# Optimization experiments

Hardware: AMD Instinct MI355X
Metric: run time of the kernel (lower is better)

The kernel has to match this reference:

```python
import jax, jax.numpy as jnp
import numpy as np

N_NODES = 50000
N_EDGES = 800000
N_GRAPHS = 512
IN_DIM = 128
HIDDEN = 64
N_CLASSES = 2


def gcn_conv(x, W, b, src, dst, n_nodes):
    """PyG GCNConv: add self-loops, symmetric deg^-1/2 normalization,
    linear transform then scatter-add aggregation at the target nodes."""
    xw = x @ W  # [N, out]
    loop = jnp.arange(n_nodes)
    s = jnp.concatenate([src, loop])  # sources incl. self-loops
    d = jnp.concatenate([dst, loop])  # targets incl. self-loops
    deg = jax.ops.segment_sum(jnp.ones(s.shape, xw.dtype), d, num_segments=n_nodes)
    dinv = jax.lax.rsqrt(jnp.where(deg > 0, deg, 1.0))
    norm = dinv[s] * dinv[d]  # [E+N]
    out = jax.ops.segment_sum(xw[s] * norm[:, None], d, num_segments=n_nodes)
    return out + b


def setup_inputs() -> dict:
    key = jax.random.key(0)
    ks = jax.random.split(key, 9)
    x = jax.random.normal(ks[0], (N_NODES, IN_DIM), dtype=jnp.float32)
    edge_index = jax.random.randint(ks[1], (2, N_EDGES), 0, N_NODES)
    batch = jnp.sort(jax.random.randint(ks[2], (N_NODES,), 0, N_GRAPHS))
    def glorot(k, fi, fo):
        return jax.random.normal(k, (fi, fo), dtype=jnp.float32) * (1.0 / np.sqrt(fi))
    W1 = glorot(ks[3], IN_DIM, HIDDEN)
    W2 = glorot(ks[4], HIDDEN, HIDDEN)
    W3 = glorot(ks[5], HIDDEN, N_CLASSES)
    b1 = jnp.zeros((HIDDEN,), jnp.float32)
    b2 = jnp.zeros((HIDDEN,), jnp.float32)
    b3 = jnp.zeros((N_CLASSES,), jnp.float32)
    return {"x": x, "edge_index": edge_index, "batch": batch,
            "W1": W1, "b1": b1, "W2": W2, "b2": b2, "W3": W3, "b3": b3}


def reference(x, edge_index, batch, W1, b1, W2, b2, W3, b3):
    # Eval mode: F.dropout(training=False) is identity.
    src, dst = edge_index[0], edge_index[1]
    z = jax.nn.relu(gcn_conv(x, W1, b1, src, dst, N_NODES))
    z = jax.nn.relu(gcn_conv(z, W2, b2, src, dst, N_NODES))
    z = gcn_conv(z, W3, b3, src, dst, N_NODES)  # [N, 2]
    # global_mean_pool over graph ids (only the last pooling result is returned)
    s = jax.ops.segment_sum(z, batch, num_segments=N_GRAPHS)
    cnt = jax.ops.segment_sum(jnp.ones((N_NODES,), z.dtype), batch, num_segments=N_GRAPHS)
    return s / jnp.clip(cnt, 1.0)[:, None]
```

## Files before the change

kernel.cpp:

```cpp
#include <hip/hip_runtime.h>
#include <hip/hip_bf16.h>

#define N_NODES   50000
#define N_EDGES   800000
#define N_GRAPHS  512
#define IN_DIM    128
#define HIDDEN    64
#define NPAD      50176
#define NBLK      196
#define SHARD_BLOCKS 1024

__global__ __launch_bounds__(256) void k_degi_sh(const int* __restrict__ dst,
                                                 int* __restrict__ degi) {
    const int shard = blockIdx.x & 7;
    const int blk   = blockIdx.x >> 3;
    const int nthr  = (SHARD_BLOCKS >> 3) * 256;
    for (int e = blk * 256 + threadIdx.x; e < N_EDGES; e += nthr) {
        int d = dst[e];
        if (((d >> 4) & 7) == shard) atomicAdd(&degi[d], 1);
    }
}

__global__ __launch_bounds__(256) void k_dinv(const int* __restrict__ degi,
                                              float* __restrict__ dinv) {
    int i = blockIdx.x * 256 + threadIdx.x;
    if (i < N_NODES) dinv[i] = rsqrtf((float)degi[i] + 1.0f);
}

__global__ __launch_bounds__(256) void k_scan_block(const int* __restrict__ degi,
                                                    int* __restrict__ offs,
                                                    int* __restrict__ bsum) {
    __shared__ int sh[256];
    int tid = threadIdx.x;
    int i = blockIdx.x * 256 + tid;
    int v = degi[i];
    sh[tid] = v;
    __syncthreads();
    #pragma unroll
    for (int off = 1; off < 256; off <<= 1) {
        int t = (tid >= off) ? sh[tid - off] : 0;
        __syncthreads();
        sh[tid] += t;
        __syncthreads();
    }
    offs[i] = sh[tid] - v;
    if (tid == 255) bsum[blockIdx.x] = sh[tid];
}

__global__ __launch_bounds__(256) void k_scan_bsum(int* __restrict__ bsum,
                                                   int* __restrict__ boff) {
    __shared__ int sh[256];
    int tid = threadIdx.x;
    int v = (tid < NBLK) ? bsum[tid] : 0;
    sh[tid] = v;
    __syncthreads();
    #pragma unroll
    for (int off = 1; off < 256; off <<= 1) {
        int t = (tid >= off) ? sh[tid - off] : 0;
        __syncthreads();
        sh[tid] += t;
        __syncthreads();
    }
    if (tid < NBLK) boff[tid] = sh[tid] - v;
}

__global__ __launch_bounds__(256) void k_scan_add(int* __restrict__ offs,
                                                  const int* __restrict__ boff,
                                                  int* __restrict__ cnt) {
    int i = blockIdx.x * 256 + threadIdx.x;
    int v = offs[i] + boff[blockIdx.x];
    offs[i] = v;
    cnt[i]  = v;
}

__global__ __launch_bounds__(256) void k_fill_sh(const int* __restrict__ src,
                                                 const int* __restrict__ dst,
                                                 int* __restrict__ cnt,
                                                 int* __restrict__ csr_src) {
    const int shard = blockIdx.x & 7;
    const int blk   = blockIdx.x >> 3;
    const int nthr  = (SHARD_BLOCKS >> 3) * 256;
    for (int e = blk * 256 + threadIdx.x; e < N_EDGES; e += nthr) {
        int d = dst[e];
        int s = src[e];
        if (((d >> 4) & 7) == shard) {
            int pos = atomicAdd(&cnt[d], 1);
            csr_src[pos] = s;
        }
    }
}

template <int K, bool RELU_IN>
__global__ __launch_bounds__(256) void k_gemm64t(const float* __restrict__ A,
                                                 const float* __restrict__ W,
                                                 const float* __restrict__ bin,
                                                 const float* __restrict__ dinv,
                                                 float* __restrict__ out) {
    __shared__ float sA[64][65];
    __shared__ float sW[64][64];
    __shared__ float sB[64];

    const int tid = threadIdx.x;
    const int rowBase = blockIdx.x * 64;
    const int c0 = (tid & 15) * 4;
    const int r0 = (tid >> 4) * 4;

    if (RELU_IN && tid < 64) sB[tid] = bin[tid];

    float acc[4][4];
    #pragma unroll
    for (int j = 0; j < 4; ++j)
        #pragma unroll
        for (int c = 0; c < 4; ++c) acc[j][c] = 0.0f;

    for (int kc = 0; kc < K; kc += 64) {
        __syncthreads();
        #pragma unroll
        for (int p = 0; p < 4; ++p) {
            int i = p * 256 + tid;
            int k  = i >> 4;
            int cq = i & 15;
            *reinterpret_cast<float4*>(&sW[k][cq * 4]) =
                *reinterpret_cast<const float4*>(&W[(size_t)(kc + k) * 64 + cq * 4]);
        }
        #pragma unroll
        for (int p = 0; p < 4; ++p) {
            int i = p * 256 + tid;
            int row = i >> 4;
            int kq  = i & 15;
            int gr = rowBase + row;
            float4 v = make_float4(0.f, 0.f, 0.f, 0.f);
            if (gr < N_NODES)
                v = *reinterpret_cast<const float4*>(&A[(size_t)gr * K + kc + kq * 4]);
            if (RELU_IN) {
                v.x = fmaxf(v.x + sB[kq * 4 + 0], 0.f);
                v.y = fmaxf(v.y + sB[kq * 4 + 1], 0.f);
                v.z = fmaxf(v.z + sB[kq * 4 + 2], 0.f);
                v.w = fmaxf(v.w + sB[kq * 4 + 3], 0.f);
            }
            sA[row][kq * 4 + 0] = v.x;
            sA[row][kq * 4 + 1] = v.y;
            sA[row][kq * 4 + 2] = v.z;
            sA[row][kq * 4 + 3] = v.w;
        }
        __syncthreads();

        #pragma unroll 8
        for (int k = 0; k < 64; ++k) {
            float4 w4 = *reinterpret_cast<const float4*>(&sW[k][c0]);
            float a0 = sA[r0 + 0][k];
            float a1 = sA[r0 + 1][k];
            float a2 = sA[r0 + 2][k];
            float a3 = sA[r0 + 3][k];
            acc[0][0] = fmaf(a0, w4.x, acc[0][0]);
            acc[0][1] = fmaf(a0, w4.y, acc[0][1]);
            acc[0][2] = fmaf(a0, w4.z, acc[0][2]);
            acc[0][3] = fmaf(a0, w4.w, acc[0][3]);
            acc[1][0] = fmaf(a1, w4.x, acc[1][0]);
            acc[1][1] = fmaf(a1, w4.y, acc[1][1]);
            acc[1][2] = fmaf(a1, w4.z, acc[1][2]);
            acc[1][3] = fmaf(a1, w4.w, acc[1][3]);
            acc[2][0] = fmaf(a2, w4.x, acc[2][0]);
            acc[2][1] = fmaf(a2, w4.y, acc[2][1]);
            acc[2][2] = fmaf(a2, w4.z, acc[2][2]);
            acc[2][3] = fmaf(a2, w4.w, acc[2][3]);
            acc[3][0] = fmaf(a3, w4.x, acc[3][0]);
            acc[3][1] = fmaf(a3, w4.y, acc[3][1]);
            acc[3][2] = fmaf(a3, w4.z, acc[3][2]);
            acc[3][3] = fmaf(a3, w4.w, acc[3][3]);
        }
    }

    #pragma unroll
    for (int j = 0; j < 4; ++j) {
        int gr = rowBase + r0 + j;
        if (gr < N_NODES) {
            float di = dinv[gr];
            float4 o;
            o.x = di * acc[j][0];
            o.y = di * acc[j][1];
            o.z = di * acc[j][2];
            o.w = di * acc[j][3];
            *reinterpret_cast<float4*>(&out[(size_t)gr * 64 + c0]) = o;
        }
    }
}

__global__ __launch_bounds__(256) void k_gemm2(const float* __restrict__ A,
                                               const float* __restrict__ W3,
                                               const float* __restrict__ b2,
                                               const float* __restrict__ dinv,
                                               float* __restrict__ out) {
    __shared__ float sW[128];
    __shared__ float sB[64];
    int tid = threadIdx.x;
    if (tid < 128) sW[tid] = W3[tid];
    if (tid < 64)  sB[tid] = b2[tid];
    __syncthreads();
    int i = blockIdx.x * 256 + tid;
    if (i >= N_NODES) return;
    float a0 = 0.f, a1 = 0.f;
    const float* row = A + (size_t)i * 64;
    #pragma unroll
    for (int k = 0; k < 64; k += 4) {
        float4 v = *reinterpret_cast<const float4*>(row + k);
        float z;
        z = fmaxf(v.x + sB[k + 0], 0.f); a0 = fmaf(z, sW[(k+0)*2+0], a0); a1 = fmaf(z, sW[(k+0)*2+1], a1);
        z = fmaxf(v.y + sB[k + 1], 0.f); a0 = fmaf(z, sW[(k+1)*2+0], a0); a1 = fmaf(z, sW[(k+1)*2+1], a1);
        z = fmaxf(v.z + sB[k + 2], 0.f); a0 = fmaf(z, sW[(k+2)*2+0], a0); a1 = fmaf(z, sW[(k+2)*2+1], a1);
        z = fmaxf(v.w + sB[k + 3], 0.f); a0 = fmaf(z, sW[(k+3)*2+0], a0); a1 = fmaf(z, sW[(k+3)*2+1], a1);
    }
    float di = dinv[i];
    out[i * 2 + 0] = di * a0;
    out[i * 2 + 1] = di * a1;
}

__global__ __launch_bounds__(256) void k_gather64(const int* __restrict__ csr_src,
                                                  const int* __restrict__ offs,
                                                  const int* __restrict__ degi,
                                                  const float* __restrict__ dinv,
                                                  const float* __restrict__ yw,
                                                  float* __restrict__ agg) {
    int gid  = blockIdx.x * 256 + threadIdx.x;
    int node = gid >> 6;
    int lane = threadIdx.x & 63;
    if (node >= N_NODES) return;
    float acc = yw[(size_t)node * 64 + lane];
    int beg = offs[node];
    int n   = degi[node];
    int j = 0;
    for (; j + 7 < n; j += 8) {
        int s[8];
        #pragma unroll
        for (int u = 0; u < 8; ++u) s[u] = csr_src[beg + j + u];
        float v[8];
        #pragma unroll
        for (int u = 0; u < 8; ++u) v[u] = yw[(size_t)s[u] * 64 + lane];
        #pragma unroll
        for (int u = 0; u < 8; ++u) acc += v[u];
    }
    for (; j < n; ++j) {
        int s = csr_src[beg + j];
        acc += yw[(size_t)s * 64 + lane];
    }
    agg[(size_t)node * 64 + lane] = dinv[node] * acc;
}

__global__ __launch_bounds__(256) void k_gather2pool(const int* __restrict__ csr_src,
                                                     const int* __restrict__ offs,
                                                     const int* __restrict__ degi,
                                                     const float* __restrict__ dinv,
                                                     const float* __restrict__ yw,
                                                     const int* __restrict__ batch,
                                                     float* __restrict__ psum,
                                                     float* __restrict__ pcnt) {
    __shared__ float ls0[N_GRAPHS];
    __shared__ float ls1[N_GRAPHS];
    __shared__ float lc [N_GRAPHS];
    int tid = threadIdx.x;
    #pragma unroll
    for (int g = tid; g < N_GRAPHS; g += 256) {
        ls0[g] = 0.f; ls1[g] = 0.f; lc[g] = 0.f;
    }
    __syncthreads();

    int node = blockIdx.x * 256 + tid;
    if (node < N_NODES) {
        float2 v = *reinterpret_cast<const float2*>(&yw[(size_t)node * 2]);
        float a0 = v.x, a1 = v.y;
        int beg = offs[node];
        int n   = degi[node];
        for (int j = 0; j < n; ++j) {
            int s = csr_src[beg + j];
            float2 u = *reinterpret_cast<const float2*>(&yw[(size_t)s * 2]);
            a0 += u.x;
            a1 += u.y;
        }
        float di = dinv[node];
        int g = batch[node];
        atomicAdd(&ls0[g], di * a0);
        atomicAdd(&ls1[g], di * a1);
        atomicAdd(&lc [g], 1.0f);
    }
    __syncthreads();

    #pragma unroll
    for (int g = tid; g < N_GRAPHS; g += 256) {
        float c = lc[g];
        if (c != 0.0f) {
            atomicAdd(&psum[g * 2 + 0], ls0[g]);
            atomicAdd(&psum[g * 2 + 1], ls1[g]);
            atomicAdd(&pcnt[g], c);
        }
    }
}

__global__ __launch_bounds__(256) void k_final(const float* __restrict__ psum,
                                               const float* __restrict__ pcnt,
                                               const float* __restrict__ b3,
                                               float* __restrict__ out) {
    int g = blockIdx.x * 256 + threadIdx.x;
    if (g >= N_GRAPHS) return;
    float c  = pcnt[g];
    float cc = fmaxf(c, 1.0f);
    out[g * 2 + 0] = (psum[g * 2 + 0] + c * b3[0]) / cc;
    out[g * 2 + 1] = (psum[g * 2 + 1] + c * b3[1]) / cc;
}

extern "C" void kernel_launch(void* const* d_in, const int* in_sizes, int n_in,
                              void* d_out, int out_size, void* d_ws, size_t ws_size,
                              hipStream_t stream) {
    const float* x     = (const float*)d_in[0];
    const int*   ei    = (const int*)d_in[1];
    const int*   batch = (const int*)d_in[2];
    const float* W1    = (const float*)d_in[3];
    const float* b1    = (const float*)d_in[4];
    const float* W2    = (const float*)d_in[5];
    const float* b2    = (const float*)d_in[6];
    const float* W3    = (const float*)d_in[7];
    const float* b3    = (const float*)d_in[8];
    const int* src = ei;
    const int* dst = ei + N_EDGES;

    float* ws   = (float*)d_ws;
    float* dinv = ws;
    int*   degi = (int*)(dinv + NPAD);
    int*   offs = degi + NPAD;
    int*   cnt  = offs + NPAD;
    int*   bsum = cnt + NPAD;
    int*   boff = bsum + 256;
    int*   csr  = boff + 256;
    float* xw   = (float*)(csr + N_EDGES);
    float* agg  = xw + (size_t)N_NODES * 64;
    float* psum = agg + (size_t)N_NODES * 64;
    float* pcnt = psum + 1024;
    float* out  = (float*)d_out;

    hipMemsetAsync(degi, 0, NPAD * sizeof(int), stream);
    hipMemsetAsync(psum, 0, (1024 + 512) * sizeof(float), stream);

    k_degi_sh<<<SHARD_BLOCKS, 256, 0, stream>>>(dst, degi);
    k_dinv<<<(N_NODES + 255) / 256, 256, 0, stream>>>(degi, dinv);
    k_scan_block<<<NBLK, 256, 0, stream>>>(degi, offs, bsum);
    k_scan_bsum<<<1, 256, 0, stream>>>(bsum, boff);
    k_scan_add<<<NBLK, 256, 0, stream>>>(offs, boff, cnt);
    k_fill_sh<<<SHARD_BLOCKS, 256, 0, stream>>>(src, dst, cnt, csr);

    k_gemm64t<128, false><<<(N_NODES + 63) / 64, 256, 0, stream>>>(x, W1, nullptr, dinv, xw);
    k_gather64<<<(N_NODES * 64) / 256, 256, 0, stream>>>(csr, offs, degi, dinv, xw, agg);

    k_gemm64t<64, true><<<(N_NODES + 63) / 64, 256, 0, stream>>>(agg, W2, b1, dinv, xw);
    k_gather64<<<(N_NODES * 64) / 256, 256, 0, stream>>>(csr, offs, degi, dinv, xw, agg);

    k_gemm2<<<(N_NODES + 255) / 256, 256, 0, stream>>>(agg, W3, b2, dinv, xw);
    k_gather2pool<<<(N_NODES + 255) / 256, 256, 0, stream>>>(csr, offs, degi, dinv, xw,
                                                             batch, psum, pcnt);

    k_final<<<(N_GRAPHS + 255) / 256, 256, 0, stream>>>(psum, pcnt, b3, out);
}
```

Measured before the change: 294.5 us.

## Fuse neighbor gathers with following dense transforms and fold dinv into scan

The layer-1 gather is merged with the layer-2 GEMM. Each block aggregates 64 nodes into shared memory and applies bias and ReLU there, then multiplies by W2. The layer-2 gather is merged with the 64x2 projection by W3 through a wave-level shuffle reduction. The dinv computation moves into the block scan kernel. This cuts three kernel launches and the round trips of the 64-wide aggregate buffers through global memory, but the fused gather+GEMM kernel has only about 782 blocks, with each wave doing 16 serial node gathers, so latency hiding may suffer.

Measured after the change: 314.3 us. 6.7% more time.

```diff
diff --git a/kernel.cpp b/kernel.cpp
--- a/kernel.cpp
+++ b/kernel.cpp
@@ -21,19 +21,15 @@
     }
 }
 
-__global__ __launch_bounds__(256) void k_dinv(const int* __restrict__ degi,
-                                              float* __restrict__ dinv) {
-    int i = blockIdx.x * 256 + threadIdx.x;
-    if (i < N_NODES) dinv[i] = rsqrtf((float)degi[i] + 1.0f);
-}
-
 __global__ __launch_bounds__(256) void k_scan_block(const int* __restrict__ degi,
                                                     int* __restrict__ offs,
-                                                    int* __restrict__ bsum) {
+                                                    int* __restrict__ bsum,
+                                                    float* __restrict__ dinv) {
     __shared__ int sh[256];
     int tid = threadIdx.x;
     int i = blockIdx.x * 256 + tid;
     int v = degi[i];
+    dinv[i] = rsqrtf((float)v + 1.0f);
     sh[tid] = v;
     __syncthreads();
     #pragma unroll
@@ -82,30 +78,25 @@
     const int nthr  = (SHARD_BLOCKS >> 3) * 256;
     for (int e = blk * 256 + threadIdx.x; e < N_EDGES; e += nthr) {
         int d = dst[e];
-        int s = src[e];
         if (((d >> 4) & 7) == shard) {
             int pos = atomicAdd(&cnt[d], 1);
-            csr_src[pos] = s;
-        }
-    }
-}
-
-template <int K, bool RELU_IN>
+            csr_src[pos] = src[e];
+        }
+    }
+}
+
+template <int K>
 __global__ __launch_bounds__(256) void k_gemm64t(const float* __restrict__ A,
                                                  const float* __restrict__ W,
-                                                 const float* __restrict__ bin,
                                                  const float* __restrict__ dinv,
                                                  float* __restrict__ out) {
     __shared__ float sA[64][65];
     __shared__ float sW[64][64];
-    __shared__ float sB[64];
 
     const int tid = threadIdx.x;
     const int rowBase = blockIdx.x * 64;
     const int c0 = (tid & 15) * 4;
     const int r0 = (tid >> 4) * 4;
-
-    if (RELU_IN && tid < 64) sB[tid] = bin[tid];
 
     float acc[4][4];
     #pragma unroll
@@ -132,12 +123,6 @@
             float4 v = make_float4(0.f, 0.f, 0.f, 0.f);
             if (gr < N_NODES)
                 v = *reinterpret_cast<const float4*>(&A[(size_t)gr * K + kc + kq * 4]);
-            if (RELU_IN) {
-                v.x = fmaxf(v.x + sB[kq * 4 + 0], 0.f);
-                v.y = fmaxf(v.y + sB[kq * 4 + 1], 0.f);
-                v.z = fmaxf(v.z + sB[kq * 4 + 2], 0.f);
-                v.w = fmaxf(v.w + sB[kq * 4 + 3], 0.f);
-            }
             sA[row][kq * 4 + 0] = v.x;
             sA[row][kq * 4 + 1] = v.y;
             sA[row][kq * 4 + 2] = v.z;
@@ -186,64 +171,162 @@
     }
 }
 
-__global__ __launch_bounds__(256) void k_gemm2(const float* __restrict__ A,
-                                               const float* __restrict__ W3,
-                                               const float* __restrict__ b2,
-                                               const float* __restrict__ dinv,
-                                               float* __restrict__ out) {
+__global__ __launch_bounds__(256) void k_gg(const int* __restrict__ csr_src,
+                                            const int* __restrict__ offs,
+                                            const int* __restrict__ degi,
+                                            const float* __restrict__ dinv,
+                                            const float* __restrict__ yw_in,
+                                            const float* __restrict__ bin,
+                                            const float* __restrict__ W,
+                                            float* __restrict__ out) {
+    __shared__ float sA[64][65];
+    __shared__ float sW[64][64];
+    __shared__ float sB[64];
+
+    const int tid = threadIdx.x;
+    const int rowBase = blockIdx.x * 64;
+
+    #pragma unroll
+    for (int p = 0; p < 4; ++p) {
+        int i = p * 256 + tid;
+        int k  = i >> 4;
+        int cq = i & 15;
+        *reinterpret_cast<float4*>(&sW[k][cq * 4]) =
+            *reinterpret_cast<const float4*>(&W[(size_t)k * 64 + cq * 4]);
+    }
+    if (tid < 64) sB[tid] = bin[tid];
+    __syncthreads();
+
+    const int wave = tid >> 6;
+    const int lane = tid & 63;
+    for (int j = 0; j < 16; ++j) {
+        int r = wave * 16 + j;
+        int node = rowBase + r;
+        float val = 0.0f;
+        if (node < N_NODES) {
+            float acc = yw_in[(size_t)node * 64 + lane];
+            int beg = offs[node];
+            int n   = degi[node];
+            int q = 0;
+            for (; q + 7 < n; q += 8) {
+                int s[8];
+                #pragma unroll
+                for (int u = 0; u < 8; ++u) s[u] = csr_src[beg + q + u];
+                float v[8];
+                #pragma unroll
+                for (int u = 0; u < 8; ++u) v[u] = yw_in[(size_t)s[u] * 64 + lane];
+                #pragma unroll
+                for (int u = 0; u < 8; ++u) acc += v[u];
+            }
+            for (; q < n; ++q) {
+                int s = csr_src[beg + q];
+                acc += yw_in[(size_t)s * 64 + lane];
+            }
+            val = fmaxf(dinv[node] * acc + sB[lane], 0.0f);
+        }
+        sA[r][lane] = val;
+    }
+    __syncthreads();
+
+    const int c0 = (tid & 15) * 4;
+    const int r0 = (tid >> 4) * 4;
+    float acc[4][4];
+    #pragma unroll
+    for (int j = 0; j < 4; ++j)
+        #pragma unroll
+        for (int c = 0; c < 4; ++c) acc[j][c] = 0.0f;
+
+    #pragma unroll 8
+    for (int k = 0; k < 64; ++k) {
+        float4 w4 = *reinterpret_cast<const float4*>(&sW[k][c0]);
+        float a0 = sA[r0 + 0][k];
+        float a1 = sA[r0 + 1][k];
+        float a2 = sA[r0 + 2][k];
+        float a3 = sA[r0 + 3][k];
+        acc[0][0] = fmaf(a0, w4.x, acc[0][0]);
+        acc[0][1] = fmaf(a0, w4.y, acc[0][1]);
+        acc[0][2] = fmaf(a0, w4.z, acc[0][2]);
+        acc[0][3] = fmaf(a0, w4.w, acc[0][3]);
+        acc[1][0] = fmaf(a1, w4.x, acc[1][0]);
+        acc[1][1] = fmaf(a1, w4.y, acc[1][1]);
+        acc[1][2] = fmaf(a1, w4.z, acc[1][2]);
+        acc[1][3] = fmaf(a1, w4.w, acc[1][3]);
+        acc[2][0] = fmaf(a2, w4.x, acc[2][0]);
+        acc[2][1] = fmaf(a2, w4.y, acc[2][1]);
+        acc[2][2] = fmaf(a2, w4.z, acc[2][2]);
+        acc[2][3] = fmaf(a2, w4.w, acc[2][3]);
+        acc[3][0] = fmaf(a3, w4.x, acc[3][0]);
+        acc[3][1] = fmaf(a3, w4.y, acc[3][1]);
+        acc[3][2] = fmaf(a3, w4.z, acc[3][2]);
+        acc[3][3] = fmaf(a3, w4.w, acc[3][3]);
+    }
+
+    #pragma unroll
+    for (int j = 0; j < 4; ++j) {
+        int gr = rowBase + r0 + j;
+        if (gr < N_NODES) {
+            float di = dinv[gr];
+            float4 o;
+            o.x = di * acc[j][0];
+            o.y = di * acc[j][1];
+            o.z = di * acc[j][2];
+            o.w = di * acc[j][3];
+            *reinterpret_cast<float4*>(&out[(size_t)gr * 64 + c0]) = o;
+        }
+    }
+}
+
+__global__ __launch_bounds__(256) void k_gyw3(const int* __restrict__ csr_src,
+                                              const int* __restrict__ offs,
+                                              const int* __restrict__ degi,
+                                              const float* __restrict__ dinv,
+                                              const float* __restrict__ yw_in,
+                                              const float* __restrict__ b2,
+                                              const float* __restrict__ W3,
+                                              float* __restrict__ yw3) {
     __shared__ float sW[128];
     __shared__ float sB[64];
     int tid = threadIdx.x;
     if (tid < 128) sW[tid] = W3[tid];
     if (tid < 64)  sB[tid] = b2[tid];
     __syncthreads();
-    int i = blockIdx.x * 256 + tid;
-    if (i >= N_NODES) return;
-    float a0 = 0.f, a1 = 0.f;
-    const float* row = A + (size_t)i * 64;
-    #pragma unroll
-    for (int k = 0; k < 64; k += 4) {
-        float4 v = *reinterpret_cast<const float4*>(row + k);
-        float z;
-        z = fmaxf(v.x + sB[k + 0], 0.f); a0 = fmaf(z, sW[(k+0)*2+0], a0); a1 = fmaf(z, sW[(k+0)*2+1], a1);
-        z = fmaxf(v.y + sB[k + 1], 0.f); a0 = fmaf(z, sW[(k+1)*2+0], a0); a1 = fmaf(z, sW[(k+1)*2+1], a1);
-        z = fmaxf(v.z + sB[k + 2], 0.f); a0 = fmaf(z, sW[(k+2)*2+0], a0); a1 = fmaf(z, sW[(k+2)*2+1], a1);
-        z = fmaxf(v.w + sB[k + 3], 0.f); a0 = fmaf(z, sW[(k+3)*2+0], a0); a1 = fmaf(z, sW[(k+3)*2+1], a1);
-    }
-    float di = dinv[i];
-    out[i * 2 + 0] = di * a0;
-    out[i * 2 + 1] = di * a1;
-}
-
-__global__ __launch_bounds__(256) void k_gather64(const int* __restrict__ csr_src,
-                                                  const int* __restrict__ offs,
-                                                  const int* __restrict__ degi,
-                                                  const float* __restrict__ dinv,
-                                                  const float* __restrict__ yw,
-                                                  float* __restrict__ agg) {
-    int gid  = blockIdx.x * 256 + threadIdx.x;
-    int node = gid >> 6;
-    int lane = threadIdx.x & 63;
+
+    int node = blockIdx.x * 4 + (tid >> 6);
+    int lane = tid & 63;
     if (node >= N_NODES) return;
-    float acc = yw[(size_t)node * 64 + lane];
+
+    float acc = yw_in[(size_t)node * 64 + lane];
     int beg = offs[node];
     int n   = degi[node];
-    int j = 0;
-    for (; j + 7 < n; j += 8) {
+    int q = 0;
+    for (; q + 7 < n; q += 8) {
         int s[8];
         #pragma unroll
-        for (int u = 0; u < 8; ++u) s[u] = csr_src[beg + j + u];
+        for (int u = 0; u < 8; ++u) s[u] = csr_src[beg + q + u];
         float v[8];
         #pragma unroll
-        for (int u = 0; u < 8; ++u) v[u] = yw[(size_t)s[u] * 64 + lane];
+        for (int u = 0; u < 8; ++u) v[u] = yw_in[(size_t)s[u] * 64 + lane];
         #pragma unroll
         for (int u = 0; u < 8; ++u) acc += v[u];
     }
-    for (; j < n; ++j) {
-        int s = csr_src[beg + j];
-        acc += yw[(size_t)s * 64 + lane];
-    }
-    agg[(size_t)node * 64 + lane] = dinv[node] * acc;
+    for (; q < n; ++q) {
+        int s = csr_src[beg + q];
+        acc += yw_in[(size_t)s * 64 + lane];
+    }
+
+    float z  = fmaxf(dinv[node] * acc + sB[lane], 0.0f);
+    float p0 = z * sW[lane * 2 + 0];
+    float p1 = z * sW[lane * 2 + 1];
+    #pragma unroll
+    for (int off = 32; off >= 1; off >>= 1) {
+        p0 += __shfl_xor(p0, off);
+        p1 += __shfl_xor(p1, off);
+    }
+    if (lane == 0) {
+        float di = dinv[node];
+        yw3[(size_t)node * 2 + 0] = di * p0;
+        yw3[(size_t)node * 2 + 1] = di * p1;
+    }
 }
 
 __global__ __launch_bounds__(256) void k_gather2pool(const int* __restrict__ csr_src,
@@ -340,21 +423,18 @@
     hipMemsetAsync(psum, 0, (1024 + 512) * sizeof(float), stream);
 
     k_degi_sh<<<SHARD_BLOCKS, 256, 0, stream>>>(dst, degi);
-    k_dinv<<<(N_NODES + 255) / 256, 256, 0, stream>>>(degi, dinv);
-    k_scan_block<<<NBLK, 256, 0, stream>>>(degi, offs, bsum);
+    k_scan_block<<<NBLK, 256, 0, stream>>>(degi, offs, bsum, dinv);
     k_scan_bsum<<<1, 256, 0, stream>>>(bsum, boff);
     k_scan_add<<<NBLK, 256, 0, stream>>>(offs, boff, cnt);
     k_fill_sh<<<SHARD_BLOCKS, 256, 0, stream>>>(src, dst, cnt, csr);
 
-    k_gemm64t<128, false><<<(N_NODES + 63) / 64, 256, 0, stream>>>(x, W1, nullptr, dinv, xw);
-    k_gather64<<<(N_NODES * 64) / 256, 256, 0, stream>>>(csr, offs, degi, dinv, xw, agg);
-
-    k_gemm64t<64, true><<<(N_NODES + 63) / 64, 256, 0, stream>>>(agg, W2, b1, dinv, xw);
-    k_gather64<<<(N_NODES * 64) / 256, 256, 0, stream>>>(csr, offs, degi, dinv, xw, agg);
-
-    k_gemm2<<<(N_NODES + 255) / 256, 256, 0, stream>>>(agg, W3, b2, dinv, xw);
+    k_gemm64t<128><<<(N_NODES + 63) / 64, 256, 0, stream>>>(x, W1, dinv, xw);
+
+    k_gg<<<(N_NODES + 63) / 64, 256, 0, stream>>>(csr, offs, degi, dinv, xw, b1, W2, agg);
+
+    k_gyw3<<<(N_NODES + 3) / 4, 256, 0, stream>>>(csr, offs, degi, dinv, agg, b2, W3, xw);
+
     k_gather2pool<<<(N_NODES + 255) / 256, 256, 0, stream>>>(csr, offs, degi, dinv, xw,
                                                              batch, psum, pcnt);
-
     k_final<<<(N_GRAPHS + 255) / 256, 256, 0, stream>>>(psum, pcnt, b3, out);
 }
```
